# Optimization experiments

Measured on AMD Instinct MI355X. Metric: run time of the kernel, lower is better.

Reference implementation:

```python
import jax, jax.numpy as jnp
import numpy as np

B, N, DQ, DK, DV = 8, 2048, 1024, 1024, 1024

def setup_inputs() -> dict:
    key = jax.random.key(0)
    kx, kq, kk, kv = jax.random.split(key, 4)
    x = jax.random.normal(kx, (B, N, DQ), dtype=jnp.float32)
    # nn.Linear(dim_q, dim_k, bias=False) weights: [out, in]
    s = 1.0 / np.sqrt(DQ)
    Wq = jax.random.uniform(kq, (DK, DQ), jnp.float32, -s, s)
    Wk = jax.random.uniform(kk, (DK, DQ), jnp.float32, -s, s)
    Wv = jax.random.uniform(kv, (DV, DQ), jnp.float32, -s, s)
    return {"x": x, "Wq": Wq, "Wk": Wk, "Wv": Wv}

def reference(x, Wq, Wk, Wv):
    batch, n, _ = x.shape
    q = jnp.einsum('bnd,kd->bnk', x, Wq)  # [B,n,DK]
    k = jnp.einsum('bnd,kd->bnk', x, Wk)  # [B,n,DK]
    v = jnp.einsum('bnd,vd->bnv', x, Wv)  # [B,n,DV]
    norm = 1.0 / jnp.sqrt(jnp.asarray(Wq.shape[0], jnp.float32))
    dist = jnp.einsum('bik,bjk->bij', q, k) * norm  # [B,n,n]
    causal = jnp.tril(jnp.ones((n, n), dtype=bool))
    dist = jnp.where(causal[None, :, :], dist, jnp.float32(-1e20))
    dist = jax.nn.softmax(dist, axis=-1)
    att = jnp.einsum('bij,bjv->biv', dist, v)  # [B,n,DV]
    return att
```

## Files before the change

kernel.cpp:

```cpp
#include <hip/hip_runtime.h>
#include <hip/hip_bf16.h>

#define BM 128
#define BN 128
#define BK 32
#define TILE_ELEMS (BM * BK)

typedef __attribute__((ext_vector_type(4))) float floatx4;
typedef __bf16 bf16x8 __attribute__((ext_vector_type(8)));
typedef unsigned int u32;
typedef unsigned short u16;

typedef __attribute__((address_space(1))) const u32 g_u32;
typedef __attribute__((address_space(3))) u32 l_u32;

__device__ __forceinline__ u16 f32_to_bf16(float f) {
    union { float f; u32 u; } x{f};
    u32 u = x.u;
    u32 r = (u + 0x7fffu + ((u >> 16) & 1u)) >> 16;
    return (u16)r;
}

__device__ __forceinline__ float bf16_bits_to_f32(u32 hi_bits) {
    union { u32 u; float f; } x{hi_bits};
    return x.f;
}

__device__ __forceinline__ void stage_tile(const u16* gbase, int ld, u16* lds, int tid) {
#pragma unroll
    for (int it = 0; it < 2; ++it) {
        int flat = it * 2048 + tid * 8;
        int row = flat >> 5;
        int col = flat & 31;
        const u16* g = gbase + (long)row * ld + col;
        __builtin_amdgcn_global_load_lds((g_u32*)g, (l_u32*)(&lds[flat]), 16, 0, 0);
    }
}

template<bool OUT_BF16>
__device__ __forceinline__ void gemm_body(
    const u16* __restrict__ Ab, const u16* __restrict__ Bb, void* __restrict__ Cb,
    int lda, int ldb, long ldc, int m0, int n0, int nkt, float scale,
    u16* As, u16* Bs)
{
    int tid = threadIdx.x;

    const u16* Arow = Ab + (long)m0 * lda;
    const u16* Brow = Bb + (long)n0 * ldb;

    stage_tile(Arow, lda, As, tid);
    stage_tile(Brow, ldb, Bs, tid);

    int wave = tid >> 6, lane = tid & 63;
    int wr = (wave >> 1) * 64, wc = (wave & 1) * 64;
    int lrow = lane & 15, quad = lane >> 4;

    floatx4 acc[4][4] = {};
    const int aoff = (wr + lrow) * BK + quad * 8;
    const int boff = (wc + lrow) * BK + quad * 8;

    for (int kt = 0; kt < nkt; ++kt) {
        __syncthreads();
        bf16x8 af[4], bfr[4];
#pragma unroll
        for (int i = 0; i < 4; ++i) {
            af[i]  = *(const bf16x8*)&As[aoff + i * 16 * BK];
            bfr[i] = *(const bf16x8*)&Bs[boff + i * 16 * BK];
        }
#pragma unroll
        for (int mi = 0; mi < 4; ++mi)
#pragma unroll
            for (int ni = 0; ni < 4; ++ni)
                acc[mi][ni] = __builtin_amdgcn_mfma_f32_16x16x32_bf16(af[mi], bfr[ni], acc[mi][ni], 0, 0, 0);
        __syncthreads();
        if (kt + 1 < nkt) {
            stage_tile(Arow + (kt + 1) * BK, lda, As, tid);
            stage_tile(Brow + (kt + 1) * BK, ldb, Bs, tid);
        }
    }

    long crow0 = m0 + wr + quad * 4;
    int  ccol0 = n0 + wc + lrow;
#pragma unroll
    for (int mi = 0; mi < 4; ++mi) {
#pragma unroll
        for (int ni = 0; ni < 4; ++ni) {
#pragma unroll
            for (int r = 0; r < 4; ++r) {
                long row = crow0 + mi * 16 + r;
                long col = ccol0 + ni * 16;
                float v = acc[mi][ni][r] * scale;
                if (OUT_BF16)
                    ((u16*)Cb)[row * ldc + col] = f32_to_bf16(v);
                else
                    ((float*)Cb)[row * ldc + col] = v;
            }
        }
    }
}

__global__ __launch_bounds__(256)
void qkv_gemm(const u16* __restrict__ A, const u16* __restrict__ B, u16* __restrict__ C)
{
    __shared__ u16 As[TILE_ELEMS];
    __shared__ u16 Bs[TILE_ELEMS];
    int xcd = blockIdx.x, i = blockIdx.y;
    int mt = xcd * 16 + (i & 15);
    int nt = i >> 4;
    gemm_body<true>(A, B, C, 1024, 1024, 3072,
                    mt * BM, nt * BN, 32, 1.0f, As, Bs);
}

__global__ __launch_bounds__(256)
void s_gemm(const u16* __restrict__ QKVi, u16* __restrict__ P)
{
    __shared__ u16 As[TILE_ELEMS];
    __shared__ u16 Bs[TILE_ELEMS];
    int b = blockIdx.x, u = blockIdx.y, v = blockIdx.z;
    int mt, nt;
    if (u <= v) { mt = v; nt = u; } else { mt = 15 - v; nt = u - v - 1; }
    const u16* Ab = QKVi + (long)b * 2048 * 3072;
    const u16* Bb = Ab + 1024;
    gemm_body<true>(Ab, Bb, P + (long)b * 2048 * 2048, 3072, 3072, 2048,
                    mt * BM, nt * BN, 32, 0.03125f, As, Bs);
}

__global__ __launch_bounds__(256)
void pv_gemm(const u16* __restrict__ P, const u16* __restrict__ Vt, float* __restrict__ O)
{
    __shared__ u16 As[TILE_ELEMS];
    __shared__ u16 Bs[TILE_ELEMS];
    int b = blockIdx.x, nt = blockIdx.y, mt = blockIdx.z;
    const u16* Ab = P + (long)b * 2048 * 2048;
    const u16* Bb = Vt + (long)b * 2048;
    gemm_body<false>(Ab, Bb, O + (long)b * 2048 * 1024, 2048, 16384, 1024,
                     mt * BM, nt * BN, mt * 4 + 4, 1.0f, As, Bs);
}

__global__ __launch_bounds__(256)
void cvt_f32_bf16(const float* __restrict__ src, u16* __restrict__ dst, long n)
{
    long idx = ((long)blockIdx.x * 256 + threadIdx.x) << 2;
    if (idx >= n) return;
    float4 f = *(const float4*)(src + idx);
    ushort4 o;
    o.x = f32_to_bf16(f.x); o.y = f32_to_bf16(f.y);
    o.z = f32_to_bf16(f.z); o.w = f32_to_bf16(f.w);
    *(ushort4*)(dst + idx) = o;
}

__global__ __launch_bounds__(256)
void cvt_w3(const float* __restrict__ Wq, const float* __restrict__ Wk,
            const float* __restrict__ Wv, u16* __restrict__ dst)
{
    int which = blockIdx.x >> 10;
    const float* src = which == 0 ? Wq : (which == 1 ? Wk : Wv);
    long base = (long)(blockIdx.x & 1023) * 1024 + threadIdx.x * 4;
    float4 f = *(const float4*)(src + base);
    ushort4 o;
    o.x = f32_to_bf16(f.x); o.y = f32_to_bf16(f.y);
    o.z = f32_to_bf16(f.z); o.w = f32_to_bf16(f.w);
    *(ushort4*)(dst + (long)which * 1048576 + base) = o;
}

__global__ __launch_bounds__(256)
void transpose_v(const u16* __restrict__ QKVi, u16* __restrict__ Vt)
{
    __shared__ u16 tile[64][64 + 8];
    int t0 = blockIdx.x * 64;
    int d0 = blockIdx.y * 64;
    int tid = threadIdx.x;
    int lr = tid >> 3, lc = (tid & 7) * 8;
#pragma unroll
    for (int p = 0; p < 2; ++p) {
        int tok = lr + p * 32;
        const u16* src = QKVi + (long)(t0 + tok) * 3072 + 2048 + d0 + lc;
        *(uint4*)&tile[tok][lc] = *(const uint4*)src;
    }
    __syncthreads();
#pragma unroll
    for (int p = 0; p < 2; ++p) {
        int dq = lr + p * 32;
        u16 vals[8];
#pragma unroll
        for (int i = 0; i < 8; ++i) vals[i] = tile[lc + i][dq];
        *(uint4*)(Vt + (long)(d0 + dq) * 16384 + t0 + lc) = *(const uint4*)vals;
    }
}

__global__ __launch_bounds__(256)
void softmax_causal(u16* __restrict__ P)
{
    __shared__ float red[8];
    long rowg = blockIdx.x;
    int i = (int)(rowg & 2047);
    u16* prow = P + (rowg << 11);
    int tid = threadIdx.x;
    int j0 = tid << 3;

    uint4 rv = *(const uint4*)(prow + j0);
    u32 w[4] = {rv.x, rv.y, rv.z, rv.w};
    float x[8];
#pragma unroll
    for (int t = 0; t < 4; ++t) {
        x[2 * t]     = bf16_bits_to_f32(w[t] << 16);
        x[2 * t + 1] = bf16_bits_to_f32(w[t] & 0xffff0000u);
    }
#pragma unroll
    for (int e = 0; e < 8; ++e)
        if (j0 + e > i) x[e] = -1e30f;

    float m = x[0];
#pragma unroll
    for (int e = 1; e < 8; ++e) m = fmaxf(m, x[e]);
#pragma unroll
    for (int o = 32; o; o >>= 1) m = fmaxf(m, __shfl_xor(m, o, 64));
    if ((tid & 63) == 0) red[tid >> 6] = m;
    __syncthreads();
    m = fmaxf(fmaxf(red[0], red[1]), fmaxf(red[2], red[3]));

    float e8[8], s = 0.f;
#pragma unroll
    for (int e = 0; e < 8; ++e) { e8[e] = __expf(x[e] - m); s += e8[e]; }
#pragma unroll
    for (int o = 32; o; o >>= 1) s += __shfl_xor(s, o, 64);
    if ((tid & 63) == 0) red[4 + (tid >> 6)] = s;
    __syncthreads();
    s = red[4] + red[5] + red[6] + red[7];
    float inv = 1.0f / s;

    u32 outw[4];
#pragma unroll
    for (int t = 0; t < 4; ++t) {
        u32 lo = f32_to_bf16(e8[2 * t] * inv);
        u32 hi = f32_to_bf16(e8[2 * t + 1] * inv);
        outw[t] = lo | (hi << 16);
    }
    uint4 ov; ov.x = outw[0]; ov.y = outw[1]; ov.z = outw[2]; ov.w = outw[3];
    *(uint4*)(prow + j0) = ov;
}

extern "C" void kernel_launch(void* const* d_in, const int* in_sizes, int n_in,
                              void* d_out, int out_size, void* d_ws, size_t ws_size,
                              hipStream_t stream)
{
    const int B = 8, N = 2048, D = 1024;
    const long MT = (long)B * N;
    const long nX = MT * D;
    const long nW = (long)D * D;

    const float* x  = (const float*)d_in[0];
    const float* Wq = (const float*)d_in[1];
    const float* Wk = (const float*)d_in[2];
    const float* Wv = (const float*)d_in[3];
    float* out = (float*)d_out;

    u16* wb   = (u16*)d_ws;
    u16* xb   = wb + 3 * nW;
    u16* QKVi = xb + nX;
    u16* P    = QKVi + 3 * nX;
    u16* Vt   = xb;

    cvt_f32_bf16<<<(int)(nX / 1024), 256, 0, stream>>>(x, xb, nX);
    cvt_w3<<<3072, 256, 0, stream>>>(Wq, Wk, Wv, wb);

    qkv_gemm<<<dim3(8, 384, 1), 256, 0, stream>>>(xb, wb, QKVi);

    transpose_v<<<dim3(256, 16, 1), 256, 0, stream>>>(QKVi, Vt);

    s_gemm<<<dim3(8, 17, 8), 256, 0, stream>>>(QKVi, P);

    softmax_causal<<<(int)MT, 256, 0, stream>>>(P);

    pv_gemm<<<dim3(8, 8, 16), 256, 0, stream>>>(P, Vt, out);
}
```

Measured before the change: 422.1 us.

## Fuse causal softmax into score and PV GEMM epilogues via row sums

```diff
diff --git a/kernel.cpp b/kernel.cpp
--- a/kernel.cpp
+++ b/kernel.cpp
@@ -19,11 +19,6 @@
     u32 u = x.u;
     u32 r = (u + 0x7fffu + ((u >> 16) & 1u)) >> 16;
     return (u16)r;
-}
-
-__device__ __forceinline__ float bf16_bits_to_f32(u32 hi_bits) {
-    union { u32 u; float f; } x{hi_bits};
-    return x.f;
 }
 
 __device__ __forceinline__ void stage_tile(const u16* gbase, int ld, u16* lds, int tid) {
@@ -37,11 +32,11 @@
     }
 }
 
-template<bool OUT_BF16>
+template<bool OUT_BF16, int MODE>
 __device__ __forceinline__ void gemm_body(
     const u16* __restrict__ Ab, const u16* __restrict__ Bb, void* __restrict__ Cb,
     int lda, int ldb, long ldc, int m0, int n0, int nkt, float scale,
-    u16* As, u16* Bs)
+    u16* As, u16* Bs, float* lsum)
 {
     int tid = threadIdx.x;
 
@@ -84,16 +79,32 @@
 #pragma unroll
     for (int mi = 0; mi < 4; ++mi) {
 #pragma unroll
-        for (int ni = 0; ni < 4; ++ni) {
-#pragma unroll
-            for (int r = 0; r < 4; ++r) {
-                long row = crow0 + mi * 16 + r;
+        for (int r = 0; r < 4; ++r) {
+            long row = crow0 + mi * 16 + r;
+            float rs = 0.f;
+            float linv = 1.f;
+            if (MODE == 2) linv = 1.0f / lsum[row];
+#pragma unroll
+            for (int ni = 0; ni < 4; ++ni) {
                 long col = ccol0 + ni * 16;
                 float v = acc[mi][ni][r] * scale;
-                if (OUT_BF16)
-                    ((u16*)Cb)[row * ldc + col] = f32_to_bf16(v);
-                else
-                    ((float*)Cb)[row * ldc + col] = v;
+                if (MODE == 1) {
+                    float e = (col > row) ? 0.f : __expf(v);
+                    ((u16*)Cb)[row * ldc + col] = f32_to_bf16(e);
+                    rs += e;
+                } else if (MODE == 2) {
+                    ((float*)Cb)[row * ldc + col] = v * linv;
+                } else {
+                    if (OUT_BF16) ((u16*)Cb)[row * ldc + col] = f32_to_bf16(v);
+                    else          ((float*)Cb)[row * ldc + col] = v;
+                }
+            }
+            if (MODE == 1) {
+                rs += __shfl_xor(rs, 1, 16);
+                rs += __shfl_xor(rs, 2, 16);
+                rs += __shfl_xor(rs, 4, 16);
+                rs += __shfl_xor(rs, 8, 16);
+                if (lrow == 0) atomicAdd(&lsum[row], rs);
             }
         }
     }
@@ -107,12 +118,12 @@
     int xcd = blockIdx.x, i = blockIdx.y;
     int mt = xcd * 16 + (i & 15);
     int nt = i >> 4;
-    gemm_body<true>(A, B, C, 1024, 1024, 3072,
-                    mt * BM, nt * BN, 32, 1.0f, As, Bs);
-}
-
-__global__ __launch_bounds__(256)
-void s_gemm(const u16* __restrict__ QKVi, u16* __restrict__ P)
+    gemm_body<true, 0>(A, B, C, 1024, 1024, 3072,
+                       mt * BM, nt * BN, 32, 1.0f, As, Bs, nullptr);
+}
+
+__global__ __launch_bounds__(256)
+void s_gemm(const u16* __restrict__ QKVi, u16* __restrict__ P, float* __restrict__ lsum)
 {
     __shared__ u16 As[TILE_ELEMS];
     __shared__ u16 Bs[TILE_ELEMS];
@@ -121,20 +132,22 @@
     if (u <= v) { mt = v; nt = u; } else { mt = 15 - v; nt = u - v - 1; }
     const u16* Ab = QKVi + (long)b * 2048 * 3072;
     const u16* Bb = Ab + 1024;
-    gemm_body<true>(Ab, Bb, P + (long)b * 2048 * 2048, 3072, 3072, 2048,
-                    mt * BM, nt * BN, 32, 0.03125f, As, Bs);
-}
-
-__global__ __launch_bounds__(256)
-void pv_gemm(const u16* __restrict__ P, const u16* __restrict__ Vt, float* __restrict__ O)
+    gemm_body<true, 1>(Ab, Bb, P + (long)b * 2048 * 2048, 3072, 3072, 2048,
+                       mt * BM, nt * BN, 32, 0.03125f, As, Bs, lsum + b * 2048);
+}
+
+__global__ __launch_bounds__(256)
+void pv_gemm(const u16* __restrict__ P, const u16* __restrict__ Vt,
+             float* __restrict__ O, const float* __restrict__ lsum)
 {
     __shared__ u16 As[TILE_ELEMS];
     __shared__ u16 Bs[TILE_ELEMS];
     int b = blockIdx.x, nt = blockIdx.y, mt = blockIdx.z;
     const u16* Ab = P + (long)b * 2048 * 2048;
     const u16* Bb = Vt + (long)b * 2048;
-    gemm_body<false>(Ab, Bb, O + (long)b * 2048 * 1024, 2048, 16384, 1024,
-                     mt * BM, nt * BN, mt * 4 + 4, 1.0f, As, Bs);
+    gemm_body<false, 2>(Ab, Bb, O + (long)b * 2048 * 1024, 2048, 16384, 1024,
+                        mt * BM, nt * BN, mt * 4 + 4, 1.0f, As, Bs,
+                        (float*)lsum + b * 2048);
 }
 
 __global__ __launch_bounds__(256)
@@ -188,58 +201,6 @@
     }
 }
 
-__global__ __launch_bounds__(256)
-void softmax_causal(u16* __restrict__ P)
-{
-    __shared__ float red[8];
-    long rowg = blockIdx.x;
-    int i = (int)(rowg & 2047);
-    u16* prow = P + (rowg << 11);
-    int tid = threadIdx.x;
-    int j0 = tid << 3;
-
-    uint4 rv = *(const uint4*)(prow + j0);
-    u32 w[4] = {rv.x, rv.y, rv.z, rv.w};
-    float x[8];
-#pragma unroll
-    for (int t = 0; t < 4; ++t) {
-        x[2 * t]     = bf16_bits_to_f32(w[t] << 16);
-        x[2 * t + 1] = bf16_bits_to_f32(w[t] & 0xffff0000u);
-    }
-#pragma unroll
-    for (int e = 0; e < 8; ++e)
-        if (j0 + e > i) x[e] = -1e30f;
-
-    float m = x[0];
-#pragma unroll
-    for (int e = 1; e < 8; ++e) m = fmaxf(m, x[e]);
-#pragma unroll
-    for (int o = 32; o; o >>= 1) m = fmaxf(m, __shfl_xor(m, o, 64));
-    if ((tid & 63) == 0) red[tid >> 6] = m;
-    __syncthreads();
-    m = fmaxf(fmaxf(red[0], red[1]), fmaxf(red[2], red[3]));
-
-    float e8[8], s = 0.f;
-#pragma unroll
-    for (int e = 0; e < 8; ++e) { e8[e] = __expf(x[e] - m); s += e8[e]; }
-#pragma unroll
-    for (int o = 32; o; o >>= 1) s += __shfl_xor(s, o, 64);
-    if ((tid & 63) == 0) red[4 + (tid >> 6)] = s;
-    __syncthreads();
-    s = red[4] + red[5] + red[6] + red[7];
-    float inv = 1.0f / s;
-
-    u32 outw[4];
-#pragma unroll
-    for (int t = 0; t < 4; ++t) {
-        u32 lo = f32_to_bf16(e8[2 * t] * inv);
-        u32 hi = f32_to_bf16(e8[2 * t + 1] * inv);
-        outw[t] = lo | (hi << 16);
-    }
-    uint4 ov; ov.x = outw[0]; ov.y = outw[1]; ov.z = outw[2]; ov.w = outw[3];
-    *(uint4*)(prow + j0) = ov;
-}
-
 extern "C" void kernel_launch(void* const* d_in, const int* in_sizes, int n_in,
                               void* d_out, int out_size, void* d_ws, size_t ws_size,
                               hipStream_t stream)
@@ -260,17 +221,17 @@
     u16* QKVi = xb + nX;
     u16* P    = QKVi + 3 * nX;
     u16* Vt   = xb;
+    float* lsum = (float*)wb;
 
     cvt_f32_bf16<<<(int)(nX / 1024), 256, 0, stream>>>(x, xb, nX);
     cvt_w3<<<3072, 256, 0, stream>>>(Wq, Wk, Wv, wb);
 
     qkv_gemm<<<dim3(8, 384, 1), 256, 0, stream>>>(xb, wb, QKVi);
 
+    hipMemsetAsync(lsum, 0, (size_t)B * N * sizeof(float), stream);
     transpose_v<<<dim3(256, 16, 1), 256, 0, stream>>>(QKVi, Vt);
 
-    s_gemm<<<dim3(8, 17, 8), 256, 0, stream>>>(QKVi, P);
-
-    softmax_causal<<<(int)MT, 256, 0, stream>>>(P);
-
-    pv_gemm<<<dim3(8, 8, 16), 256, 0, stream>>>(P, Vt, out);
-}
+    s_gemm<<<dim3(8, 17, 8), 256, 0, stream>>>(QKVi, P, lsum);
+
+    pv_gemm<<<dim3(8, 8, 16), 256, 0, stream>>>(P, Vt, out, lsum);
+}
```

Result: no change. 420.1 us (-0.5%).
